# Kernel optimization log

Measured on AMD Instinct MI355X. Metric: run time of the kernel, lower is better.

The kernel has to match this reference:

```python
import jax, jax.numpy as jnp
import numpy as np

D = 40       # d_model
SL = 10      # sequenceLength
AN = 268     # actionNum
B = 8192     # batch


def relu6(x):
    return jnp.clip(x, 0.0, 6.0)


def setup_inputs() -> dict:
    key = jax.random.key(0)
    ks = jax.random.split(key, 16)
    s = 1.0 / np.sqrt(D)
    X = jax.random.randint(ks[0], (B, SL, 4), 0, AN)
    t1 = jax.random.randint(ks[1], (B, SL - 1), 0, 7)
    t2 = jax.random.randint(ks[2], (B, SL - 1), 0, 8)
    # per-step Linear(1, D): weight [D,1] -> store as [SL-1, D]; kaiming-uniform bound 1/sqrt(1)=1
    Ew = jax.random.uniform(ks[3], (SL - 1, D), minval=-1.0, maxval=1.0)
    Eb = jax.random.uniform(ks[4], (SL - 1, D), minval=-1.0, maxval=1.0)
    Qw = jax.random.uniform(ks[5], (SL - 1, D, D), minval=-s, maxval=s)
    Qb = jax.random.uniform(ks[6], (SL - 1, D), minval=-s, maxval=s)
    Lw = jax.random.uniform(ks[7], (SL - 1, D * D, D), minval=-s, maxval=s)
    Lb = jax.random.uniform(ks[8], (SL - 1, D * D), minval=-s, maxval=s)
    Mw = jax.random.uniform(ks[9], (SL - 1, D, D), minval=-s, maxval=s)
    Mb = jax.random.uniform(ks[10], (SL - 1, D), minval=-s, maxval=s)
    Tw = jax.random.uniform(ks[11], (AN, D), minval=-s, maxval=s)
    Tb = jax.random.uniform(ks[12], (AN,), minval=-s, maxval=s)
    emb = jax.random.normal(ks[13], (AN, D))
    return dict(X=X, t1=t1, t2=t2, Ew=Ew, Eb=Eb, Qw=Qw, Qb=Qb, Lw=Lw, Lb=Lb,
                Mw=Mw, Mb=Mb, Tw=Tw, Tb=Tb, emb=emb)


def reference(X, t1, t2, Ew, Eb, Qw, Qb, Lw, Lb, Mw, Mb, Tw, Tb, emb):
    b = X.shape[0]
    t = (t1 * 8 + t2).astype(jnp.float32)          # [B, SL-1]
    ae = emb[X[:, :SL - 1, 3]]                     # [B, SL-1, D]

    def step(carry, xs):
        h0, p0 = carry
        ew, eb, qw, qb, lw, lb, mw, mb, ti, ei = xs
        # E(t_i) + Q(p0), both [B, D]
        p1 = relu6(ti[:, None] * ew[None, :] + eb + p0 @ qw.T + qb)
        # hypernetwork-generated per-sample matrix [B, D, D]
        jt = relu6(p1 @ lw.T + lb).reshape(b, D, D)
        tt = jnp.einsum('bd,bde->be', h0, jt)
        h1 = relu6(ei @ mw.T + mb + tt)
        return (h1, p1), None

    xs = (Ew, Eb, Qw, Qb, Lw, Lb, Mw, Mb, t.T, jnp.swapaxes(ae, 0, 1))
    init = (jnp.zeros((b, D), jnp.float32), jnp.zeros((b, D), jnp.float32))
    (h0, _), _ = jax.lax.scan(step, init, xs)
    return h0 @ Tw.T + Tb                          # [B, AN]
```

## Files before the change

### kernel.cpp

```cpp
#include <hip/hip_runtime.h>

#define DD 40
#define SLM1 9
#define ANUM 268
#define MB 32

typedef __attribute__((ext_vector_type(8))) short short8;
typedef __attribute__((ext_vector_type(4))) float f32x4;
typedef __attribute__((ext_vector_type(16))) float f32x16;

#define WS_LWF ((size_t)0)
#define WS_LWT ((size_t)552960)
#define WS_QW  ((size_t)691200)
#define WS_MW  ((size_t)718848)
#define WS_TW  ((size_t)746496)

__device__ __forceinline__ unsigned short f2bf(float f){
  unsigned int u = __float_as_uint(f);
  u += 0x7FFFu + ((u >> 16) & 1u);
  return (unsigned short)(u >> 16);
}
__device__ __forceinline__ float relu6f(float v){
  return fminf(fmaxf(v, 0.0f), 6.0f);
}

__device__ __forceinline__ f32x16 mfma3(short8 a0, short8 a1, short8 a2,
                                        short8 b0, short8 b1, short8 b2){
  f32x16 c = {0,0,0,0,0,0,0,0,0,0,0,0,0,0,0,0};
  c = __builtin_amdgcn_mfma_f32_32x32x16_bf16(a0, b0, c, 0, 0, 0);
  c = __builtin_amdgcn_mfma_f32_32x32x16_bf16(a1, b1, c, 0, 0, 0);
  c = __builtin_amdgcn_mfma_f32_32x32x16_bf16(a2, b2, c, 0, 0, 0);
  return c;
}

__global__ __launch_bounds__(512)
void prep_frags(const float* __restrict__ Qw, const float* __restrict__ Lw,
                const float* __restrict__ Mw, const float* __restrict__ Tw,
                const float* __restrict__ Ew, const float* __restrict__ Eb,
                const float* __restrict__ Qb, const float* __restrict__ Lb,
                const float* __restrict__ Mb, const float* __restrict__ Tb,
                unsigned short* __restrict__ ws)
{
  const int bid = blockIdx.x, tid = threadIdx.x;
  if (bid < 360){
    int s = bid / 40, d = bid - s*40;
    unsigned short* dst = ws + WS_LWF + (size_t)bid*1536;
    const float* W = Lw + (size_t)s*64000;
    const float* bv = Lb + (size_t)s*1600;
    for (int i = tid; i < 1536; i += 512){
      int kf = i >> 9, q = i & 511, l = q >> 3, j = q & 7;
      int k = kf*16 + ((l >> 5) << 3) + j;
      int e = l & 31;
      int n = d*DD + e;
      float v = 0.f;
      if (k < DD) v = W[n*DD + k];
      else if (k == DD) v = bv[n];
      dst[i] = f2bf(v);
    }
  } else if (bid < 450){
    int t = bid - 360;
    int s = t / 10, tt = t - s*10;
    unsigned short* dst = ws + WS_LWT + (size_t)t*1536;
    const float* W = Lw + (size_t)s*64000;
    const float* bv = Lb + (size_t)s*1600;
    for (int i = tid; i < 1536; i += 512){
      int kf = i >> 9, q = i & 511, l = q >> 3, j = q & 7;
      int k = kf*16 + ((l >> 5) << 3) + j;
      int c = l & 31;
      int d = 4*tt + (c >> 3);
      int e = 32 + (c & 7);
      int n = d*DD + e;
      float v = 0.f;
      if (k < DD) v = W[n*DD + k];
      else if (k == DD) v = bv[n];
      dst[i] = f2bf(v);
    }
  } else if (bid < 459){
    int s = bid - 450;
    unsigned short* dst = ws + WS_QW + (size_t)s*3072;
    const float* W = Qw + (size_t)s*1600;
    for (int i = tid; i < 3072; i += 512){
      int et = i / 1536, r = i - et*1536;
      int kf = r >> 9, q = r & 511, l = q >> 3, j = q & 7;
      int k = kf*16 + ((l >> 5) << 3) + j;
      int jc = et*32 + (l & 31);
      float v = 0.f;
      if (jc < DD){
        if (k < DD) v = W[jc*DD + k];
        else if (k == DD) v = Eb[s*DD + jc] + Qb[s*DD + jc];
        else if (k == DD+1) v = Ew[s*DD + jc];
      }
      dst[i] = f2bf(v);
    }
  } else if (bid < 468){
    int s = bid - 459;
    unsigned short* dst = ws + WS_MW + (size_t)s*3072;
    const float* W = Mw + (size_t)s*1600;
    for (int i = tid; i < 3072; i += 512){
      int et = i / 1536, r = i - et*1536;
      int kf = r >> 9, q = r & 511, l = q >> 3, j = q & 7;
      int k = kf*16 + ((l >> 5) << 3) + j;
      int e = et*32 + (l & 31);
      float v = 0.f;
      if (e < DD){
        if (k < DD) v = W[e*DD + k];
        else if (k == DD) v = Mb[s*DD + e];
      }
      dst[i] = f2bf(v);
    }
  } else {
    int t = bid - 468;
    unsigned short* dst = ws + WS_TW + (size_t)t*1536;
    for (int i = tid; i < 1536; i += 512){
      int kf = i >> 9, q = i & 511, l = q >> 3, j = q & 7;
      int k = kf*16 + ((l >> 5) << 3) + j;
      int a = t*32 + (l & 31);
      float v = 0.f;
      if (a < ANUM){
        if (k < DD) v = Tw[(size_t)a*DD + k];
        else if (k == DD) v = Tb[a];
      }
      dst[i] = f2bf(v);
    }
  }
}

__global__ __launch_bounds__(512)
void star_main(const int* __restrict__ X,
               const int* __restrict__ T1,
               const int* __restrict__ T2,
               const float* __restrict__ emb,
               const unsigned short* __restrict__ ws,
               float* __restrict__ out)
{
  __shared__ __align__(16) unsigned short pbuf[2][3072];
  __shared__ __align__(16) unsigned short aebf[2][3072];
  __shared__ __align__(16) float hT[2][DD*36];
  __shared__ __align__(16) float red[8][MB*DD];
  __shared__ int   aeidx[SLM1][MB];
  __shared__ float tvtab[SLM1][MB];

  const int tid = threadIdx.x;
  const int w = __builtin_amdgcn_readfirstlane(tid >> 6);
  const int l = tid & 63;
  const int col = l & 31, half = l >> 5;
  const int row0 = blockIdx.x * MB;

  {
    unsigned int* p = (unsigned int*)&pbuf[0][0];
    for (int i = tid; i < 3072; i += 512) p[i] = 0u;
    unsigned int* a = (unsigned int*)&aebf[0][0];
    for (int i = tid; i < 3072; i += 512) a[i] = 0u;
    float* rr = &red[0][0];
    for (int i = tid; i < 8*MB*DD; i += 512) rr[i] = 0.f;
  }
  if (tid < MB*SLM1){
    int m = tid / SLM1, s = tid - m*SLM1;
    int r = row0 + m;
    aeidx[s][m] = X[(size_t)r*40 + s*4 + 3];
    tvtab[s][m] = (float)(T1[r*SLM1 + s]*8 + T2[r*SLM1 + s]);
  }
  __syncthreads();
  if (tid < MB){
    int off = 2*1024 + (tid + 32)*8;
    pbuf[0][off] = 0x3F80; pbuf[1][off] = 0x3F80;
    aebf[0][off] = 0x3F80; aebf[1][off] = 0x3F80;
    pbuf[0][off+1] = f2bf(tvtab[0][tid]);
    pbuf[1][off+1] = f2bf(tvtab[1][tid]);
  }
  if (tid < 320){
    int m = tid / 10, q4 = tid - m*10;
    float4 v4 = *(const float4*)(emb + (size_t)aeidx[0][m]*DD + q4*4);
    #pragma unroll
    for (int c2 = 0; c2 < 4; ++c2){
      int k = q4*4 + c2, kf = k >> 4, kk = k & 15;
      aebf[0][kf*1024 + (m + ((kk >> 3) << 5))*8 + (kk & 7)] = f2bf(((const float*)&v4)[c2]);
    }
  }
  __syncthreads();
  if (w < 2){
    short8 a0 = ((const short8*)&pbuf[0][0])[l];
    short8 a1 = ((const short8*)&pbuf[0][1024])[l];
    short8 a2 = ((const short8*)&pbuf[0][2048])[l];
    const unsigned short* qwb = ws + WS_QW + w*1536;
    f32x16 c = mfma3(a0, a1, a2, ((const short8*)qwb)[l],
                     ((const short8*)(qwb+512))[l], ((const short8*)(qwb+1024))[l]);
    int j = w*32 + col;
    if (j < DD){
      int kf = j >> 4, kk = j & 15;
      #pragma unroll
      for (int r = 0; r < 16; ++r){
        int m = (r & 3) + ((r >> 2) << 3) + (half << 2);
        pbuf[1][kf*1024 + (m + ((kk >> 3) << 5))*8 + (kk & 7)] = f2bf(relu6f(c[r]));
      }
    }
  }
  __syncthreads();

  short8 q00, q01, q02, q10, q11, q12;

  for (int s = 0; s < SLM1; ++s){
    const int pcur = (s + 1) & 1;
    const int hrd  = s & 1;

    float4 gv; int gm = 0, gq = 0;
    const bool dog = (s < 8) && (tid < 320);
    if (dog){
      gm = tid / 10; gq = tid - gm*10;
      gv = *(const float4*)(emb + (size_t)aeidx[s+1][gm]*DD + gq*4);
    }
    short8 pa0 = ((const short8*)&pbuf[pcur][0])[l];
    short8 pa1 = ((const short8*)&pbuf[pcur][1024])[l];
    short8 pa2 = ((const short8*)&pbuf[pcur][2048])[l];

    short8 A0, A1, A2, B0, B1, B2;

    if (s > 0){
      const float* hbase = &hT[hrd][half << 2];
      const unsigned short* lwf = ws + WS_LWF + (size_t)(s*40)*1536;

      A0 = q00; A1 = q01; A2 = q02;
      B0 = q10; B1 = q11; B2 = q12;
      f32x16 tt = {0,0,0,0,0,0,0,0,0,0,0,0,0,0,0,0};

      #pragma unroll
      for (int it = 0; it < 2; ++it){
        short8 NA0, NA1, NA2, NB0, NB1, NB2;
        if (it == 0){
          const unsigned short* fA = lwf + (size_t)(16 + w)*1536;
          NA0 = ((const short8*)fA)[l];
          NA1 = ((const short8*)(fA + 512))[l];
          NA2 = ((const short8*)(fA + 1024))[l];
          const unsigned short* fB = lwf + (size_t)(24 + w)*1536;
          NB0 = ((const short8*)fB)[l];
          NB1 = ((const short8*)(fB + 512))[l];
          NB2 = ((const short8*)(fB + 1024))[l];
        } else {
          const unsigned short* fA = lwf + (size_t)(32 + w)*1536;
          NA0 = ((const short8*)fA)[l];
          NA1 = ((const short8*)(fA + 512))[l];
          NA2 = ((const short8*)(fA + 1024))[l];
          const size_t qs = (s < 8) ? (size_t)(s + 1) : (size_t)8;
          const unsigned short* fB = (w < 6)
              ? ws + WS_LWT + (size_t)(s*10 + w)*1536
              : ws + WS_QW + qs*3072 + (size_t)(w - 6)*1536;
          NB0 = ((const short8*)fB)[l];
          NB1 = ((const short8*)(fB + 512))[l];
          NB2 = ((const short8*)(fB + 1024))[l];
        }
        f32x16 ca = {0,0,0,0,0,0,0,0,0,0,0,0,0,0,0,0};
        f32x16 cb = {0,0,0,0,0,0,0,0,0,0,0,0,0,0,0,0};
        ca = __builtin_amdgcn_mfma_f32_32x32x16_bf16(pa0, A0, ca, 0, 0, 0);
        cb = __builtin_amdgcn_mfma_f32_32x32x16_bf16(pa0, B0, cb, 0, 0, 0);
        ca = __builtin_amdgcn_mfma_f32_32x32x16_bf16(pa1, A1, ca, 0, 0, 0);
        cb = __builtin_amdgcn_mfma_f32_32x32x16_bf16(pa1, B1, cb, 0, 0, 0);
        ca = __builtin_amdgcn_mfma_f32_32x32x16_bf16(pa2, A2, ca, 0, 0, 0);
        cb = __builtin_amdgcn_mfma_f32_32x32x16_bf16(pa2, B2, cb, 0, 0, 0);
        const int dA = it*16 + w, dB = it*16 + 8 + w;
        const float* hA = hbase + dA*36;
        const float* hB = hbase + dB*36;
        #pragma unroll
        for (int g = 0; g < 4; ++g){
          f32x4 ha = *(const f32x4*)(hA + g*8);
          f32x4 hb = *(const f32x4*)(hB + g*8);
          #pragma unroll
          for (int q = 0; q < 4; ++q){
            tt[g*4+q] = fmaf(ha[q], relu6f(ca[g*4+q]), tt[g*4+q]);
            tt[g*4+q] = fmaf(hb[q], relu6f(cb[g*4+q]), tt[g*4+q]);
          }
        }
        A0 = NA0; A1 = NA1; A2 = NA2;
        B0 = NB0; B1 = NB1; B2 = NB2;
      }
      {
        f32x16 c = mfma3(pa0, pa1, pa2, A0, A1, A2);
        const float* hb = hbase + (32 + w)*36;
        #pragma unroll
        for (int g = 0; g < 4; ++g){
          f32x4 hg = *(const f32x4*)(hb + g*8);
          #pragma unroll
          for (int q = 0; q < 4; ++q)
            tt[g*4+q] = fmaf(hg[q], relu6f(c[g*4+q]), tt[g*4+q]);
        }
      }
      #pragma unroll
      for (int r = 0; r < 16; ++r){
        int m = (r & 3) + ((r >> 2) << 3) + (half << 2);
        red[w][m*DD + col] = tt[r];
      }
    }

    if (s < 8){
      const unsigned short* nl = ws + WS_LWF + (size_t)((s+1)*40)*1536;
      const unsigned short* n0 = nl + (size_t)w*1536;
      q00 = ((const short8*)n0)[l];
      q01 = ((const short8*)(n0 + 512))[l];
      q02 = ((const short8*)(n0 + 1024))[l];
      const unsigned short* n1 = nl + (size_t)(8 + w)*1536;
      q10 = ((const short8*)n1)[l];
      q11 = ((const short8*)(n1 + 512))[l];
      q12 = ((const short8*)(n1 + 1024))[l];
    }

    if (s > 0 && w < 6){
      const unsigned short* lwt = ws + WS_LWT + (size_t)(s*10)*1536;
      const float* hb0;
      f32x16 tacc = {0,0,0,0,0,0,0,0,0,0,0,0,0,0,0,0};
      {
        f32x16 c = mfma3(pa0, pa1, pa2, B0, B1, B2);
        int dt = 4*w + (col >> 3);
        hb0 = &hT[hrd][dt*36 + (half << 2)];
        #pragma unroll
        for (int g = 0; g < 4; ++g){
          f32x4 hg = *(const f32x4*)(hb0 + g*8);
          #pragma unroll
          for (int q = 0; q < 4; ++q){
            float val = hg[q]*relu6f(c[g*4+q]);
            val += __shfl_xor(val, 8);
            val += __shfl_xor(val, 16);
            tacc[g*4+q] += val;
          }
        }
      }
      if (w < 4){
        const int t2 = w + 6;
        const unsigned short* ft = lwt + (size_t)t2*1536;
        short8 t0 = ((const short8*)ft)[l];
        short8 t1 = ((const short8*)(ft + 512))[l];
        short8 t2r = ((const short8*)(ft + 1024))[l];
        f32x16 c = mfma3(pa0, pa1, pa2, t0, t1, t2r);
        int dt = 4*t2 + (col >> 3);
        const float* hb = &hT[hrd][dt*36 + (half << 2)];
        #pragma unroll
        for (int g = 0; g < 4; ++g){
          f32x4 hg = *(const f32x4*)(hb + g*8);
          #pragma unroll
          for (int q = 0; q < 4; ++q){
            float val = hg[q]*relu6f(c[g*4+q]);
            val += __shfl_xor(val, 8);
            val += __shfl_xor(val, 16);
            tacc[g*4+q] += val;
          }
        }
      }
      if (col < 8){
        #pragma unroll
        for (int r = 0; r < 16; ++r){
          int m = (r & 3) + ((r >> 2) << 3) + (half << 2);
          red[w][m*DD + 32 + col] = tacc[r];
        }
      }
    } else if (w >= 6 && s < 8){
      short8 Q0, Q1, Q2;
      if (s == 0){
        const unsigned short* qwb = ws + WS_QW + (size_t)(s+1)*3072 + (size_t)(w-6)*1536;
        Q0 = ((const short8*)qwb)[l];
        Q1 = ((const short8*)(qwb + 512))[l];
        Q2 = ((const short8*)(qwb + 1024))[l];
      } else {
        Q0 = B0; Q1 = B1; Q2 = B2;
      }
      f32x16 c = mfma3(pa0, pa1, pa2, Q0, Q1, Q2);
      int j = (w - 6)*32 + col;
      if (j < DD){
        int kf = j >> 4, kk = j & 15;
        #pragma unroll
        for (int r = 0; r < 16; ++r){
          int m = (r & 3) + ((r >> 2) << 3) + (half << 2);
          pbuf[s & 1][kf*1024 + (m + ((kk >> 3) << 5))*8 + (kk & 7)] = f2bf(relu6f(c[r]));
        }
      }
    }
    if (dog){
      unsigned short* dst = &aebf[(s+1) & 1][0];
      #pragma unroll
      for (int c2 = 0; c2 < 4; ++c2){
        int k = gq*4 + c2, kf = k >> 4, kk = k & 15;
        dst[kf*1024 + (gm + ((kk >> 3) << 5))*8 + (kk & 7)] = f2bf(((const float*)&gv)[c2]);
      }
    }
    if (s <= 6 && tid < MB)
      pbuf[s & 1][2*1024 + (tid + 32)*8 + 1] = f2bf(tvtab[s+2][tid]);
    __syncthreads();

    if (w < 2){
      short8 a0 = ((const short8*)&aebf[s & 1][0])[l];
      short8 a1 = ((const short8*)&aebf[s & 1][1024])[l];
      short8 a2 = ((const short8*)&aebf[s & 1][2048])[l];
      const unsigned short* mwb = ws + WS_MW + (size_t)s*3072 + w*1536;
      int e = w*32 + col;
      f32x16 c = {0,0,0,0,0,0,0,0,0,0,0,0,0,0,0,0};
      if (e < DD){
        #pragma unroll
        for (int r = 0; r < 16; ++r){
          int m = (r & 3) + ((r >> 2) << 3) + (half << 2);
          float acc = red[0][m*DD + e];
          #pragma unroll
          for (int dp = 1; dp < 8; ++dp) acc += red[dp][m*DD + e];
          c[r] = acc;
        }
      }
      c = __builtin_amdgcn_mfma_f32_32x32x16_bf16(a0, ((const short8*)mwb)[l], c, 0, 0, 0);
      c = __builtin_amdgcn_mfma_f32_32x32x16_bf16(a1, ((const short8*)(mwb+512))[l], c, 0, 0, 0);
      c = __builtin_amdgcn_mfma_f32_32x32x16_bf16(a2, ((const short8*)(mwb+1024))[l], c, 0, 0, 0);
      if (e < DD){
        int kf = e >> 4, kk = e & 15;
        #pragma unroll
        for (int r = 0; r < 16; ++r){
          int m = (r & 3) + ((r >> 2) << 3) + (half << 2);
          float v = relu6f(c[r]);
          hT[(s+1) & 1][e*36 + m] = v;
          if (s == SLM1-1)
            aebf[1][kf*1024 + (m + ((kk >> 3) << 5))*8 + (kk & 7)] = f2bf(v);
        }
      }
    }
    __syncthreads();
  }

  for (int t = w; t < 9; t += 8){
    short8 a0 = ((const short8*)&aebf[1][0])[l];
    short8 a1 = ((const short8*)&aebf[1][1024])[l];
    short8 a2 = ((const short8*)&aebf[1][2048])[l];
    const unsigned short* twb = ws + WS_TW + (size_t)t*1536;
    f32x16 c = mfma3(a0, a1, a2, ((const short8*)twb)[l],
                     ((const short8*)(twb+512))[l], ((const short8*)(twb+1024))[l]);
    int a = t*32 + col;
    if (a < ANUM){
      #pragma unroll
      for (int r = 0; r < 16; ++r){
        int m = (r & 3) + ((r >> 2) << 3) + (half << 2);
        out[(size_t)(row0 + m)*ANUM + a] = c[r];
      }
    }
  }
}

extern "C" void kernel_launch(void* const* d_in, const int* in_sizes, int n_in,
                              void* d_out, int out_size, void* d_ws, size_t ws_size,
                              hipStream_t stream) {
  const int*   X  = (const int*)  d_in[0];
  const int*   T1 = (const int*)  d_in[1];
  const int*   T2 = (const int*)  d_in[2];
  const float* Ew = (const float*)d_in[3];
  const float* Eb = (const float*)d_in[4];
  const float* Qw = (const float*)d_in[5];
  const float* Qb = (const float*)d_in[6];
  const float* Lw = (const float*)d_in[7];
  const float* Lb = (const float*)d_in[8];
  const float* Mw = (const float*)d_in[9];
  const float* Mb = (const float*)d_in[10];
  const float* Tw = (const float*)d_in[11];
  const float* Tb = (const float*)d_in[12];
  const float* em = (const float*)d_in[13];
  unsigned short* ws = (unsigned short*)d_ws;
  float* out = (float*)d_out;

  prep_frags<<<dim3(477), dim3(512), 0, stream>>>(Qw, Lw, Mw, Tw, Ew, Eb, Qb,
                                                  Lb, Mb, Tb, ws);
  star_main<<<dim3(8192 / MB), dim3(512), 0, stream>>>(X, T1, T2, em, ws, out);
}
```

Baseline: 55.53 us.

## Spread per-step h-update across six waves using 16x16x32 MFMA tiles

The serial h1 update stage (reduction of partial tt sums plus the Mw matmul) now runs on six waves with 16x16x32 bf16 MFMA tiles. Before, it ran on two waves with 32x32x16 tiles, so each wave now reduces only 4 rows instead of 16. The embedding operand buffer gets a new 16-row fragment layout, and the Mw weight fragments are re-laid out to match. The reduction scratch row stride is padded from 40 to 42 to ease LDS bank conflicts, and the hypernetwork MFMA loop is bracketed with s_setprio. The final projection reuses pbuf[0] for the last hidden state, which removes the old 3-fragment aebf buffer.

```diff
diff --git a/kernel.cpp b/kernel.cpp
--- a/kernel.cpp
+++ b/kernel.cpp
@@ -4,6 +4,7 @@
 #define SLM1 9
 #define ANUM 268
 #define MB 32
+#define RST2 42
 
 typedef __attribute__((ext_vector_type(8))) short short8;
 typedef __attribute__((ext_vector_type(4))) float f32x4;
@@ -31,6 +32,10 @@
   c = __builtin_amdgcn_mfma_f32_32x32x16_bf16(a1, b1, c, 0, 0, 0);
   c = __builtin_amdgcn_mfma_f32_32x32x16_bf16(a2, b2, c, 0, 0, 0);
   return c;
+}
+
+__device__ __forceinline__ int ae16_off(int m, int k){
+  return (m >> 4)*1024 + (k >> 5)*512 + (((k & 31) >> 3) << 7) + (m & 15)*8 + (k & 7);
 }
 
 __global__ __launch_bounds__(512)
@@ -97,10 +102,9 @@
     unsigned short* dst = ws + WS_MW + (size_t)s*3072;
     const float* W = Mw + (size_t)s*1600;
     for (int i = tid; i < 3072; i += 512){
-      int et = i / 1536, r = i - et*1536;
-      int kf = r >> 9, q = r & 511, l = q >> 3, j = q & 7;
-      int k = kf*16 + ((l >> 5) << 3) + j;
-      int e = et*32 + (l & 31);
+      int et = i >> 10, r = i & 1023, kf = r >> 9, q = r & 511, l = q >> 3, j = q & 7;
+      int k = kf*32 + ((l >> 4) << 3) + j;
+      int e = et*16 + (l & 15);
       float v = 0.f;
       if (e < DD){
         if (k < DD) v = W[e*DD + k];
@@ -134,9 +138,9 @@
                float* __restrict__ out)
 {
   __shared__ __align__(16) unsigned short pbuf[2][3072];
-  __shared__ __align__(16) unsigned short aebf[2][3072];
+  __shared__ __align__(16) unsigned short aebf16[2][2048];
   __shared__ __align__(16) float hT[2][DD*36];
-  __shared__ __align__(16) float red[8][MB*DD];
+  __shared__ __align__(16) float red[8][MB*RST2];
   __shared__ int   aeidx[SLM1][MB];
   __shared__ float tvtab[SLM1][MB];
 
@@ -149,10 +153,10 @@
   {
     unsigned int* p = (unsigned int*)&pbuf[0][0];
     for (int i = tid; i < 3072; i += 512) p[i] = 0u;
-    unsigned int* a = (unsigned int*)&aebf[0][0];
-    for (int i = tid; i < 3072; i += 512) a[i] = 0u;
+    unsigned int* a = (unsigned int*)&aebf16[0][0];
+    for (int i = tid; i < 2048; i += 512) a[i] = 0u;
     float* rr = &red[0][0];
-    for (int i = tid; i < 8*MB*DD; i += 512) rr[i] = 0.f;
+    for (int i = tid; i < 8*MB*RST2; i += 512) rr[i] = 0.f;
   }
   if (tid < MB*SLM1){
     int m = tid / SLM1, s = tid - m*SLM1;
@@ -164,18 +168,17 @@
   if (tid < MB){
     int off = 2*1024 + (tid + 32)*8;
     pbuf[0][off] = 0x3F80; pbuf[1][off] = 0x3F80;
-    aebf[0][off] = 0x3F80; aebf[1][off] = 0x3F80;
     pbuf[0][off+1] = f2bf(tvtab[0][tid]);
     pbuf[1][off+1] = f2bf(tvtab[1][tid]);
+    int o16 = ae16_off(tid, 40);
+    aebf16[0][o16] = 0x3F80; aebf16[1][o16] = 0x3F80;
   }
   if (tid < 320){
     int m = tid / 10, q4 = tid - m*10;
     float4 v4 = *(const float4*)(emb + (size_t)aeidx[0][m]*DD + q4*4);
     #pragma unroll
-    for (int c2 = 0; c2 < 4; ++c2){
-      int k = q4*4 + c2, kf = k >> 4, kk = k & 15;
-      aebf[0][kf*1024 + (m + ((kk >> 3) << 5))*8 + (kk & 7)] = f2bf(((const float*)&v4)[c2]);
-    }
+    for (int c2 = 0; c2 < 4; ++c2)
+      aebf16[0][ae16_off(m, q4*4 + c2)] = f2bf(((const float*)&v4)[c2]);
   }
   __syncthreads();
   if (w < 2){
@@ -223,6 +226,7 @@
       B0 = q10; B1 = q11; B2 = q12;
       f32x16 tt = {0,0,0,0,0,0,0,0,0,0,0,0,0,0,0,0};
 
+      __builtin_amdgcn_s_setprio(1);
       #pragma unroll
       for (int it = 0; it < 2; ++it){
         short8 NA0, NA1, NA2, NB0, NB1, NB2;
@@ -283,10 +287,11 @@
             tt[g*4+q] = fmaf(hg[q], relu6f(c[g*4+q]), tt[g*4+q]);
         }
       }
+      __builtin_amdgcn_s_setprio(0);
       #pragma unroll
       for (int r = 0; r < 16; ++r){
         int m = (r & 3) + ((r >> 2) << 3) + (half << 2);
-        red[w][m*DD + col] = tt[r];
+        red[w][m*RST2 + col] = tt[r];
       }
     }
 
@@ -304,12 +309,11 @@
 
     if (s > 0 && w < 6){
       const unsigned short* lwt = ws + WS_LWT + (size_t)(s*10)*1536;
-      const float* hb0;
       f32x16 tacc = {0,0,0,0,0,0,0,0,0,0,0,0,0,0,0,0};
       {
         f32x16 c = mfma3(pa0, pa1, pa2, B0, B1, B2);
         int dt = 4*w + (col >> 3);
-        hb0 = &hT[hrd][dt*36 + (half << 2)];
+        const float* hb0 = &hT[hrd][dt*36 + (half << 2)];
         #pragma unroll
         for (int g = 0; g < 4; ++g){
           f32x4 hg = *(const f32x4*)(hb0 + g*8);
@@ -347,7 +351,7 @@
         #pragma unroll
         for (int r = 0; r < 16; ++r){
           int m = (r & 3) + ((r >> 2) << 3) + (half << 2);
-          red[w][m*DD + 32 + col] = tacc[r];
+          red[w][m*RST2 + 32 + col] = tacc[r];
         }
       }
     } else if (w >= 6 && s < 8){
@@ -372,46 +376,49 @@
       }
     }
     if (dog){
-      unsigned short* dst = &aebf[(s+1) & 1][0];
+      unsigned short* dst = &aebf16[(s+1) & 1][0];
       #pragma unroll
-      for (int c2 = 0; c2 < 4; ++c2){
-        int k = gq*4 + c2, kf = k >> 4, kk = k & 15;
-        dst[kf*1024 + (gm + ((kk >> 3) << 5))*8 + (kk & 7)] = f2bf(((const float*)&gv)[c2]);
-      }
+      for (int c2 = 0; c2 < 4; ++c2)
+        dst[ae16_off(gm, gq*4 + c2)] = f2bf(((const float*)&gv)[c2]);
     }
     if (s <= 6 && tid < MB)
       pbuf[s & 1][2*1024 + (tid + 32)*8 + 1] = f2bf(tvtab[s+2][tid]);
     __syncthreads();
 
-    if (w < 2){
-      short8 a0 = ((const short8*)&aebf[s & 1][0])[l];
-      short8 a1 = ((const short8*)&aebf[s & 1][1024])[l];
-      short8 a2 = ((const short8*)&aebf[s & 1][2048])[l];
-      const unsigned short* mwb = ws + WS_MW + (size_t)s*3072 + w*1536;
-      int e = w*32 + col;
-      f32x16 c = {0,0,0,0,0,0,0,0,0,0,0,0,0,0,0,0};
+    if (w < 6){
+      const int mt = (w >= 3) ? 1 : 0, et = w - mt*3;
+      const int lr = l & 15, lg = l >> 4;
+      const int e = et*16 + lr;
+      const int mbase = mt*16 + (lg << 2);
+      f32x4 c = {0.f, 0.f, 0.f, 0.f};
       if (e < DD){
         #pragma unroll
-        for (int r = 0; r < 16; ++r){
-          int m = (r & 3) + ((r >> 2) << 3) + (half << 2);
-          float acc = red[0][m*DD + e];
+        for (int r = 0; r < 4; ++r){
+          int m = mbase + r;
+          float acc = red[0][m*RST2 + e];
           #pragma unroll
-          for (int dp = 1; dp < 8; ++dp) acc += red[dp][m*DD + e];
+          for (int dp = 1; dp < 8; ++dp) acc += red[dp][m*RST2 + e];
           c[r] = acc;
         }
       }
-      c = __builtin_amdgcn_mfma_f32_32x32x16_bf16(a0, ((const short8*)mwb)[l], c, 0, 0, 0);
-      c = __builtin_amdgcn_mfma_f32_32x32x16_bf16(a1, ((const short8*)(mwb+512))[l], c, 0, 0, 0);
-      c = __builtin_amdgcn_mfma_f32_32x32x16_bf16(a2, ((const short8*)(mwb+1024))[l], c, 0, 0, 0);
+      const unsigned short* ab = &aebf16[s & 1][mt*1024];
+      short8 a0 = ((const short8*)ab)[l];
+      short8 a1 = ((const short8*)(ab + 512))[l];
+      const unsigned short* mwb = ws + WS_MW + (size_t)s*3072 + (size_t)et*1024;
+      short8 b0 = ((const short8*)mwb)[l];
+      short8 b1 = ((const short8*)(mwb + 512))[l];
+      c = __builtin_amdgcn_mfma_f32_16x16x32_bf16(a0, b0, c, 0, 0, 0);
+      c = __builtin_amdgcn_mfma_f32_16x16x32_bf16(a1, b1, c, 0, 0, 0);
       if (e < DD){
-        int kf = e >> 4, kk = e & 15;
-        #pragma unroll
-        for (int r = 0; r < 16; ++r){
-          int m = (r & 3) + ((r >> 2) << 3) + (half << 2);
+        #pragma unroll
+        for (int r = 0; r < 4; ++r){
+          int m = mbase + r;
           float v = relu6f(c[r]);
           hT[(s+1) & 1][e*36 + m] = v;
-          if (s == SLM1-1)
-            aebf[1][kf*1024 + (m + ((kk >> 3) << 5))*8 + (kk & 7)] = f2bf(v);
+          if (s == SLM1-1){
+            int kf = e >> 4, kk = e & 15;
+            pbuf[0][kf*1024 + (m + ((kk >> 3) << 5))*8 + (kk & 7)] = f2bf(v);
+          }
         }
       }
     }
@@ -419,9 +426,9 @@
   }
 
   for (int t = w; t < 9; t += 8){
-    short8 a0 = ((const short8*)&aebf[1][0])[l];
-    short8 a1 = ((const short8*)&aebf[1][1024])[l];
-    short8 a2 = ((const short8*)&aebf[1][2048])[l];
+    short8 a0 = ((const short8*)&pbuf[0][0])[l];
+    short8 a1 = ((const short8*)&pbuf[0][1024])[l];
+    short8 a2 = ((const short8*)&pbuf[0][2048])[l];
     const unsigned short* twb = ws + WS_TW + (size_t)t*1536;
     f32x16 c = mfma3(a0, a1, a2, ((const short8*)twb)[l],
                      ((const short8*)(twb+512))[l], ((const short8*)(twb+1024))[l]);
```

Measured after the change: 48.54 us. 1.14x faster.
